# Kernel optimization log

Measured on AMD Instinct MI355X. Metric: run time of the kernel, lower is better.

The kernel has to match this reference:

```python
import jax, jax.numpy as jnp
import numpy as np

EMBED_DIM = 768
NUM_HEADS = 12
D_K = EMBED_DIM // NUM_HEADS


def setup_inputs() -> dict:
    key = jax.random.key(0)
    ks = jax.random.split(key, 9)
    b, s, d = 4, 2048, EMBED_DIM
    scale = 1.0 / np.sqrt(d)
    x = jax.random.normal(ks[0], (b, s, d), dtype=jnp.float32)
    return {
        "x": x,
        "w_q": jax.random.normal(ks[1], (d, d), dtype=jnp.float32) * scale,
        "b_q": jnp.zeros((d,), dtype=jnp.float32),
        "w_k": jax.random.normal(ks[2], (d, d), dtype=jnp.float32) * scale,
        "b_k": jnp.zeros((d,), dtype=jnp.float32),
        "w_v": jax.random.normal(ks[3], (d, d), dtype=jnp.float32) * scale,
        "b_v": jnp.zeros((d,), dtype=jnp.float32),
        "w_o": jax.random.normal(ks[4], (d, d), dtype=jnp.float32) * scale,
        "b_o": jnp.zeros((d,), dtype=jnp.float32),
    }


def reference(x, w_q, b_q, w_k, b_k, w_v, b_v, w_o, b_o):
    b, s, d = x.shape
    h, dk = NUM_HEADS, D_K
    # projections (torch Linear: x @ W^T + b)
    q = (x @ w_q.T + b_q).reshape(b, s, h, dk).transpose(0, 2, 1, 3)
    k = (x @ w_k.T + b_k).reshape(b, s, h, dk).transpose(0, 2, 1, 3)
    v = (x @ w_v.T + b_v).reshape(b, s, h, dk).transpose(0, 2, 1, 3)
    # causal attention: full [b,h,s,s] scores as in the original
    scores = jnp.einsum("bhqd,bhkd->bhqk", q, k) / jnp.sqrt(jnp.float32(dk))
    causal = jnp.tril(jnp.ones((s, s), dtype=bool))
    scores = jnp.where(causal[None, None], scores, -jnp.inf)
    attn = jax.nn.softmax(scores, axis=-1)
    out = jnp.einsum("bhqk,bhkd->bhqd", attn, v)
    out = out.transpose(0, 2, 1, 3).reshape(b, s, h * dk)
    return out @ w_o.T + b_o
```

## Files before the change

kernel.cpp:

```cpp
#include <hip/hip_runtime.h>
#include <hip/hip_bf16.h>
#include <stdint.h>

typedef short bf16x8 __attribute__((ext_vector_type(8)));
typedef float f32x4 __attribute__((ext_vector_type(4)));
typedef unsigned short u16;


__device__ __forceinline__ u16 f2bf_bits(float f) {
    __hip_bfloat16 h = __float2bfloat16(f);
    return __builtin_bit_cast(u16, h);
}

__device__ __forceinline__ uint32_t pack2bf(float a, float b) {
    uint32_t ua = __builtin_bit_cast(uint32_t, a) + 0x8000u;
    uint32_t ub = __builtin_bit_cast(uint32_t, b) + 0x8000u;
    return __builtin_amdgcn_perm(ub, ua, 0x07060302u);
}

__device__ __forceinline__ void gld_lds16(const void* g, void* l) {
    __builtin_amdgcn_global_load_lds(
        (const __attribute__((address_space(1))) void*)g,
        (__attribute__((address_space(3))) void*)l, 16, 0, 0);
}

#define CEXP 0.18033688011112042f


__global__ __launch_bounds__(256) void cast_all_kernel(
    const float* __restrict__ x, const float* __restrict__ w0,
    const float* __restrict__ w1, const float* __restrict__ w2,
    const float* __restrict__ w3, u16* __restrict__ xb,
    u16* __restrict__ o0, u16* __restrict__ o1,
    u16* __restrict__ o2, u16* __restrict__ o3,
    const float* __restrict__ bq, const float* __restrict__ bk,
    const float* __restrict__ bv, float* __restrict__ biasf) {
    int gid = blockIdx.x * 256 + threadIdx.x;
    const float* s;
    u16* d;
    int off;
    if (gid < 1572864) {
        s = x; d = xb; off = gid;
    } else {
        int g2 = gid - 1572864;
        int which = g2 / 147456;
        off = g2 - which * 147456;
        s = which == 0 ? w0 : which == 1 ? w1 : which == 2 ? w2 : w3;
        d = which == 0 ? o0 : which == 1 ? o1 : which == 2 ? o2 : o3;
    }
    float4 v = ((const float4*)s)[off];
    ushort4 u;
    u.x = f2bf_bits(v.x); u.y = f2bf_bits(v.y);
    u.z = f2bf_bits(v.z); u.w = f2bf_bits(v.w);
    ((ushort4*)d)[off] = u;
    if (gid < 2304) {
        float bb = gid < 768 ? bq[gid] : gid < 1536 ? bk[gid - 768] : bv[gid - 1536];
        biasf[gid] = bb;
    }
}


template <int RT, int MODE>
__global__ __launch_bounds__(256) void gemm_xwt(
    const u16* __restrict__ X, const u16* __restrict__ W,
    const float* __restrict__ bias, float* __restrict__ Cf,
    u16* __restrict__ Cb, u16* __restrict__ Vt, int K, int NC) {
    constexpr int JR = RT / 32;
    __shared__ u16 lsX[RT * 64];
    __shared__ u16 lsW[128 * 64];
    const int tid = threadIdx.x;
    const int w = tid >> 6, lane = tid & 63;
    const int quad = lane >> 4, l15 = lane & 15;
    const int m0 = blockIdx.y * RT, n0 = blockIdx.x * 128;
    const int wr = (w >> 1) * (RT / 2), wc = (w & 1) * 64;
    const int rr = lane >> 3, c8 = lane & 7;

    f32x4 acc[JR][4];
    for (int j = 0; j < JR; ++j)
        for (int i = 0; i < 4; ++i) acc[j][i] = (f32x4){0.f, 0.f, 0.f, 0.f};

    const int KT = K / 64;
    for (int kt = 0; kt < KT; ++kt) {
        const int k0 = kt * 64;
        __syncthreads();
        for (int cb = w; cb < RT / 8; cb += 4) {
            int row = cb * 8 + rr;
            int cg = c8 ^ ((rr ^ cb) & 7);
            gld_lds16(X + (size_t)(m0 + row) * K + k0 + cg * 8, &lsX[cb * 512]);
        }
        for (int cb = w; cb < 16; cb += 4) {
            int row = cb * 8 + rr;
            int cg = c8 ^ ((rr ^ cb) & 7);
            gld_lds16(W + (size_t)(n0 + row) * K + k0 + cg * 8, &lsW[cb * 512]);
        }
        __syncthreads();

        for (int kk = 0; kk < 2; ++kk) {
            bf16x8 xf[JR], wf[4];
            for (int j = 0; j < JR; ++j) {
                int row = wr + j * 16 + l15;
                int slot = (kk * 4 + quad) ^ ((row ^ (row >> 3)) & 7);
                xf[j] = *(const bf16x8*)&lsX[row * 64 + slot * 8];
            }
            for (int i = 0; i < 4; ++i) {
                int row = wc + i * 16 + l15;
                int slot = (kk * 4 + quad) ^ ((row ^ (row >> 3)) & 7);
                wf[i] = *(const bf16x8*)&lsW[row * 64 + slot * 8];
            }
            for (int j = 0; j < JR; ++j)
                for (int i = 0; i < 4; ++i)
                    acc[j][i] = __builtin_amdgcn_mfma_f32_16x16x32_bf16(
                        wf[i], xf[j], acc[j][i], 0, 0, 0);
        }
    }

    const bool vtile = (MODE == 2) && (n0 >= 1536);
    for (int i = 0; i < 4; ++i) {
        int c0 = n0 + wc + i * 16 + quad * 4;
        float4 bv4 = *(const float4*)&bias[c0];
        for (int j = 0; j < JR; ++j) {
            int row = m0 + wr + j * 16 + l15;
            float v0 = acc[j][i][0] + bv4.x;
            float v1 = acc[j][i][1] + bv4.y;
            float v2 = acc[j][i][2] + bv4.z;
            float v3 = acc[j][i][3] + bv4.w;
            if (MODE == 1) {
                float4 o4 = {v0, v1, v2, v3};
                *(float4*)&Cf[(size_t)row * NC + c0] = o4;
            } else if (vtile) {
                int d = c0 - 1536;
                int bq_ = row >> 11;
                int s = row & 2047;
                int h = d >> 6, dd = d & 63;
                size_t base = ((size_t)(bq_ * 12 + h) * 64 + dd) * 2048 + s;
                Vt[base]          = f2bf_bits(v0);
                Vt[base + 2048]   = f2bf_bits(v1);
                Vt[base + 4096]   = f2bf_bits(v2);
                Vt[base + 6144]   = f2bf_bits(v3);
            } else {
                uint2 pk = {pack2bf(v0, v1), pack2bf(v2, v3)};
                *(uint2*)&Cb[(size_t)row * NC + c0] = pk;
            }
        }
    }
}


__global__ __launch_bounds__(256, 3) void attn_kernel(
    const u16* __restrict__ QKV, const u16* __restrict__ Vt, u16* __restrict__ O) {
    __shared__ u16 lsQ[128 * 64];
    __shared__ u16 lsK[64 * 64];
    __shared__ u16 lsV[64 * 64];
    __shared__ u16 lsP[4][32 * 72];

    int bx = blockIdx.x;
    int bh = bx % 48;
    int qtb = 15 - (bx / 48);
    int b = bh / 12, h = bh % 12;
    int tid = threadIdx.x, w = tid >> 6, lane = tid & 63;
    int quad = lane >> 4, l15 = lane & 15;
    int rr = lane >> 3, c8 = lane & 7;

    for (int cb = w; cb < 16; cb += 4) {
        int row = cb * 8 + rr;
        int cg = c8 ^ ((rr ^ cb) & 7);
        gld_lds16(QKV + (size_t)(b * 2048 + qtb * 128 + row) * 2304 + h * 64 + cg * 8,
                  &lsQ[cb * 512]);
    }
    __syncthreads();

    bf16x8 q0[2], q1[2];
    for (int g = 0; g < 2; ++g) {
        int rowq = g * 64 + w * 16 + l15;
        int swq = (rowq ^ (rowq >> 3)) & 7;
        q0[g] = *(const bf16x8*)&lsQ[rowq * 64 + ((0 + quad) ^ swq) * 8];
        q1[g] = *(const bf16x8*)&lsQ[rowq * 64 + ((4 + quad) ^ swq) * 8];
    }

    f32x4 oacc0[4], oacc1[4];
    for (int dt = 0; dt < 4; ++dt) {
        oacc0[dt] = (f32x4){0.f, 0.f, 0.f, 0.f};
        oacc1[dt] = (f32x4){0.f, 0.f, 0.f, 0.f};
    }
    float li0 = 0.f, li1 = 0.f;
    u16* Pw = lsP[w];
    const int qrel = w * 16 + l15;
    const int ktmax = 2 * qtb + 1;

    for (int kt = 0; kt <= ktmax; ++kt) {
        __syncthreads();
        for (int cb = w; cb < 8; cb += 4) {
            int row = cb * 8 + rr;
            int cg = c8 ^ ((rr ^ cb) & 7);
            gld_lds16(QKV + (size_t)(b * 2048 + kt * 64 + row) * 2304 + 768 + h * 64 + cg * 8,
                      &lsK[cb * 512]);
            gld_lds16(Vt + (size_t)(bh * 64 + row) * 2048 + kt * 64 + cg * 8,
                      &lsV[cb * 512]);
        }
        __syncthreads();

        const bool do0 = (kt <= 2 * qtb);

        f32x4 S0[4], S1[4];
        for (int ct = 0; ct < 4; ++ct) {
            int rowk = ct * 16 + l15;
            int swk = (rowk ^ (rowk >> 3)) & 7;
            bf16x8 k0 = *(const bf16x8*)&lsK[rowk * 64 + ((0 + quad) ^ swk) * 8];
            bf16x8 k1 = *(const bf16x8*)&lsK[rowk * 64 + ((4 + quad) ^ swk) * 8];
            f32x4 z = (f32x4){0.f, 0.f, 0.f, 0.f};
            S1[ct] = __builtin_amdgcn_mfma_f32_16x16x32_bf16(k0, q0[1], z, 0, 0, 0);
            S1[ct] = __builtin_amdgcn_mfma_f32_16x16x32_bf16(k1, q1[1], S1[ct], 0, 0, 0);
            if (do0) {
                S0[ct] = __builtin_amdgcn_mfma_f32_16x16x32_bf16(k0, q0[0], z, 0, 0, 0);
                S0[ct] = __builtin_amdgcn_mfma_f32_16x16x32_bf16(k1, q1[0], S0[ct], 0, 0, 0);
            }
        }

        if (kt == 2 * qtb) {
            for (int ct = 0; ct < 4; ++ct) {
                int kbase = ct * 16 + quad * 4;
                for (int r = 0; r < 4; ++r)
                    if (kbase + r > qrel) S0[ct][r] = -1e30f;
            }
        }
        if (kt == 2 * qtb + 1) {
            for (int ct = 0; ct < 4; ++ct) {
                int kbase = ct * 16 + quad * 4;
                for (int r = 0; r < 4; ++r)
                    if (kbase + r > qrel) S1[ct][r] = -1e30f;
            }
        }

        if (do0) {
            u16* Pr = &Pw[(size_t)l15 * 72];
            for (int ct = 0; ct < 4; ++ct) {
                float p0 = __builtin_amdgcn_exp2f(S0[ct][0] * CEXP);
                float p1 = __builtin_amdgcn_exp2f(S0[ct][1] * CEXP);
                float p2 = __builtin_amdgcn_exp2f(S0[ct][2] * CEXP);
                float p3 = __builtin_amdgcn_exp2f(S0[ct][3] * CEXP);
                li0 += (p0 + p1) + (p2 + p3);
                uint2 pk = {pack2bf(p0, p1), pack2bf(p2, p3)};
                *(uint2*)&Pr[ct * 16 + quad * 4] = pk;
            }
        }
        {
            u16* Pr = &Pw[(size_t)(16 + l15) * 72];
            for (int ct = 0; ct < 4; ++ct) {
                float p0 = __builtin_amdgcn_exp2f(S1[ct][0] * CEXP);
                float p1 = __builtin_amdgcn_exp2f(S1[ct][1] * CEXP);
                float p2 = __builtin_amdgcn_exp2f(S1[ct][2] * CEXP);
                float p3 = __builtin_amdgcn_exp2f(S1[ct][3] * CEXP);
                li1 += (p0 + p1) + (p2 + p3);
                uint2 pk = {pack2bf(p0, p1), pack2bf(p2, p3)};
                *(uint2*)&Pr[ct * 16 + quad * 4] = pk;
            }
        }

        for (int ks = 0; ks < 2; ++ks) {
            bf16x8 bp1 = *(const bf16x8*)&Pw[(size_t)(16 + l15) * 72 + ks * 32 + quad * 8];
            bf16x8 bp0;
            if (do0) bp0 = *(const bf16x8*)&Pw[(size_t)l15 * 72 + ks * 32 + quad * 8];
            for (int dt = 0; dt < 4; ++dt) {
                int rowv = dt * 16 + l15;
                int swv = (rowv ^ (rowv >> 3)) & 7;
                bf16x8 av = *(const bf16x8*)&lsV[rowv * 64 + ((ks * 4 + quad) ^ swv) * 8];
                oacc1[dt] = __builtin_amdgcn_mfma_f32_16x16x32_bf16(av, bp1, oacc1[dt], 0, 0, 0);
                if (do0)
                    oacc0[dt] = __builtin_amdgcn_mfma_f32_16x16x32_bf16(av, bp0, oacc0[dt], 0, 0, 0);
            }
        }
    }

    li0 += __shfl_xor(li0, 16, 64);
    li0 += __shfl_xor(li0, 32, 64);
    li1 += __shfl_xor(li1, 16, 64);
    li1 += __shfl_xor(li1, 32, 64);
    float inv0 = 1.0f / li0, inv1 = 1.0f / li1;

    for (int g = 0; g < 2; ++g) {
        float inv = g ? inv1 : inv0;
        f32x4* oa = g ? oacc1 : oacc0;
        int row = qtb * 128 + g * 64 + w * 16 + l15;
        for (int dt = 0; dt < 4; ++dt) {
            uint2 pk = {pack2bf(oa[dt][0] * inv, oa[dt][1] * inv),
                        pack2bf(oa[dt][2] * inv, oa[dt][3] * inv)};
            *(uint2*)&O[(size_t)(b * 2048 + row) * 768 + h * 64 + dt * 16 + quad * 4] = pk;
        }
    }
}


extern "C" void kernel_launch(void* const* d_in, const int* in_sizes, int n_in,
                              void* d_out, int out_size, void* d_ws, size_t ws_size,
                              hipStream_t stream) {
    const float* x  = (const float*)d_in[0];
    const float* wq = (const float*)d_in[1];
    const float* bq = (const float*)d_in[2];
    const float* wk = (const float*)d_in[3];
    const float* bk = (const float*)d_in[4];
    const float* wv = (const float*)d_in[5];
    const float* bv = (const float*)d_in[6];
    const float* wo = (const float*)d_in[7];
    const float* bo = (const float*)d_in[8];
    float* out = (float*)d_out;

    char* ws = (char*)d_ws;
    u16*   xb    = (u16*)(ws + 0);
    u16*   Wf    = (u16*)(ws + 12582912);
    u16*   wob   = (u16*)(ws + 16121856);
    float* biasf = (float*)(ws + 17301504);
    u16*   QKVb  = (u16*)(ws + 17310720);
    u16*   Vtw   = (u16*)(ws + 55059456);
    u16*   Ow    = (u16*)(ws + 67642368);

    cast_all_kernel<<<8448, 256, 0, stream>>>(x, wq, wk, wv, wo,
                                              xb, Wf, Wf + 589824, Wf + 1179648, wob,
                                              bq, bk, bv, biasf);

    gemm_xwt<128, 2><<<dim3(18, 64), 256, 0, stream>>>(xb, Wf, biasf, nullptr, QKVb,
                                                       Vtw, 768, 2304);
    attn_kernel<<<768, 256, 0, stream>>>(QKVb, Vtw, Ow);
    gemm_xwt<64, 1><<<dim3(6, 128), 256, 0, stream>>>(Ow, wob, bo, out, nullptr,
                                                      nullptr, 768, 768);
}
```

Baseline: 219.0 us.

## Shrink attention query tile to 64 rows and overlap K/V staging with compute

```diff
diff --git a/kernel.cpp b/kernel.cpp
--- a/kernel.cpp
+++ b/kernel.cpp
@@ -146,146 +146,117 @@
 }
 
 
-__global__ __launch_bounds__(256, 3) void attn_kernel(
+__global__ __launch_bounds__(256, 5) void attn_kernel(
     const u16* __restrict__ QKV, const u16* __restrict__ Vt, u16* __restrict__ O) {
-    __shared__ u16 lsQ[128 * 64];
     __shared__ u16 lsK[64 * 64];
     __shared__ u16 lsV[64 * 64];
-    __shared__ u16 lsP[4][32 * 72];
+    __shared__ u16 lsP[4][16 * 72];
 
     int bx = blockIdx.x;
     int bh = bx % 48;
-    int qtb = 15 - (bx / 48);
-    int b = bh / 12, h = bh % 12;
+    int qt = 31 - bx / 48;
+    int bb = bh / 12, h = bh % 12;
     int tid = threadIdx.x, w = tid >> 6, lane = tid & 63;
     int quad = lane >> 4, l15 = lane & 15;
     int rr = lane >> 3, c8 = lane & 7;
 
-    for (int cb = w; cb < 16; cb += 4) {
-        int row = cb * 8 + rr;
-        int cg = c8 ^ ((rr ^ cb) & 7);
-        gld_lds16(QKV + (size_t)(b * 2048 + qtb * 128 + row) * 2304 + h * 64 + cg * 8,
-                  &lsQ[cb * 512]);
-    }
+    const size_t kgbase = (size_t)(bb * 2048) * 2304 + 768 + (size_t)h * 64;
+    const size_t vgbase = (size_t)(bh * 64) * 2048;
+
+    auto stageK = [&](int kt) {
+        for (int cb = w; cb < 8; cb += 4) {
+            int row = cb * 8 + rr;
+            int cg = c8 ^ ((rr ^ cb) & 7);
+            gld_lds16(QKV + kgbase + (size_t)(kt * 64 + row) * 2304 + cg * 8,
+                      &lsK[cb * 512]);
+        }
+    };
+    auto stageV = [&](int kt) {
+        for (int cb = w; cb < 8; cb += 4) {
+            int row = cb * 8 + rr;
+            int cg = c8 ^ ((rr ^ cb) & 7);
+            gld_lds16(Vt + vgbase + (size_t)row * 2048 + kt * 64 + cg * 8,
+                      &lsV[cb * 512]);
+        }
+    };
+
+    const int qrow = qt * 64 + w * 16 + l15;
+    const u16* qp = QKV + (size_t)(bb * 2048 + qrow) * 2304 + (size_t)h * 64;
+    bf16x8 q0 = *(const bf16x8*)(qp + quad * 8);
+    bf16x8 q1 = *(const bf16x8*)(qp + 32 + quad * 8);
+
+    stageK(0);
+    stageV(0);
     __syncthreads();
 
-    bf16x8 q0[2], q1[2];
-    for (int g = 0; g < 2; ++g) {
-        int rowq = g * 64 + w * 16 + l15;
-        int swq = (rowq ^ (rowq >> 3)) & 7;
-        q0[g] = *(const bf16x8*)&lsQ[rowq * 64 + ((0 + quad) ^ swq) * 8];
-        q1[g] = *(const bf16x8*)&lsQ[rowq * 64 + ((4 + quad) ^ swq) * 8];
-    }
-
-    f32x4 oacc0[4], oacc1[4];
-    for (int dt = 0; dt < 4; ++dt) {
-        oacc0[dt] = (f32x4){0.f, 0.f, 0.f, 0.f};
-        oacc1[dt] = (f32x4){0.f, 0.f, 0.f, 0.f};
-    }
-    float li0 = 0.f, li1 = 0.f;
+    f32x4 oacc[4];
+    for (int dt = 0; dt < 4; ++dt) oacc[dt] = (f32x4){0.f, 0.f, 0.f, 0.f};
+    float li = 0.f;
     u16* Pw = lsP[w];
     const int qrel = w * 16 + l15;
-    const int ktmax = 2 * qtb + 1;
-
-    for (int kt = 0; kt <= ktmax; ++kt) {
-        __syncthreads();
-        for (int cb = w; cb < 8; cb += 4) {
-            int row = cb * 8 + rr;
-            int cg = c8 ^ ((rr ^ cb) & 7);
-            gld_lds16(QKV + (size_t)(b * 2048 + kt * 64 + row) * 2304 + 768 + h * 64 + cg * 8,
-                      &lsK[cb * 512]);
-            gld_lds16(Vt + (size_t)(bh * 64 + row) * 2048 + kt * 64 + cg * 8,
-                      &lsV[cb * 512]);
-        }
-        __syncthreads();
-
-        const bool do0 = (kt <= 2 * qtb);
-
-        f32x4 S0[4], S1[4];
+
+    for (int kt = 0; kt <= qt; ++kt) {
+        f32x4 S[4];
+        __builtin_amdgcn_s_setprio(1);
         for (int ct = 0; ct < 4; ++ct) {
             int rowk = ct * 16 + l15;
             int swk = (rowk ^ (rowk >> 3)) & 7;
             bf16x8 k0 = *(const bf16x8*)&lsK[rowk * 64 + ((0 + quad) ^ swk) * 8];
             bf16x8 k1 = *(const bf16x8*)&lsK[rowk * 64 + ((4 + quad) ^ swk) * 8];
             f32x4 z = (f32x4){0.f, 0.f, 0.f, 0.f};
-            S1[ct] = __builtin_amdgcn_mfma_f32_16x16x32_bf16(k0, q0[1], z, 0, 0, 0);
-            S1[ct] = __builtin_amdgcn_mfma_f32_16x16x32_bf16(k1, q1[1], S1[ct], 0, 0, 0);
-            if (do0) {
-                S0[ct] = __builtin_amdgcn_mfma_f32_16x16x32_bf16(k0, q0[0], z, 0, 0, 0);
-                S0[ct] = __builtin_amdgcn_mfma_f32_16x16x32_bf16(k1, q1[0], S0[ct], 0, 0, 0);
-            }
-        }
-
-        if (kt == 2 * qtb) {
+            S[ct] = __builtin_amdgcn_mfma_f32_16x16x32_bf16(k0, q0, z, 0, 0, 0);
+            S[ct] = __builtin_amdgcn_mfma_f32_16x16x32_bf16(k1, q1, S[ct], 0, 0, 0);
+        }
+        __builtin_amdgcn_s_setprio(0);
+
+        if (kt == qt) {
             for (int ct = 0; ct < 4; ++ct) {
                 int kbase = ct * 16 + quad * 4;
                 for (int r = 0; r < 4; ++r)
-                    if (kbase + r > qrel) S0[ct][r] = -1e30f;
-            }
-        }
-        if (kt == 2 * qtb + 1) {
-            for (int ct = 0; ct < 4; ++ct) {
-                int kbase = ct * 16 + quad * 4;
-                for (int r = 0; r < 4; ++r)
-                    if (kbase + r > qrel) S1[ct][r] = -1e30f;
-            }
-        }
-
-        if (do0) {
+                    if (kbase + r > qrel) S[ct][r] = -1e30f;
+            }
+        }
+
+        {
             u16* Pr = &Pw[(size_t)l15 * 72];
             for (int ct = 0; ct < 4; ++ct) {
-                float p0 = __builtin_amdgcn_exp2f(S0[ct][0] * CEXP);
-                float p1 = __builtin_amdgcn_exp2f(S0[ct][1] * CEXP);
-                float p2 = __builtin_amdgcn_exp2f(S0[ct][2] * CEXP);
-                float p3 = __builtin_amdgcn_exp2f(S0[ct][3] * CEXP);
-                li0 += (p0 + p1) + (p2 + p3);
+                float p0 = __builtin_amdgcn_exp2f(S[ct][0] * CEXP);
+                float p1 = __builtin_amdgcn_exp2f(S[ct][1] * CEXP);
+                float p2 = __builtin_amdgcn_exp2f(S[ct][2] * CEXP);
+                float p3 = __builtin_amdgcn_exp2f(S[ct][3] * CEXP);
+                li += (p0 + p1) + (p2 + p3);
                 uint2 pk = {pack2bf(p0, p1), pack2bf(p2, p3)};
                 *(uint2*)&Pr[ct * 16 + quad * 4] = pk;
             }
         }
-        {
-            u16* Pr = &Pw[(size_t)(16 + l15) * 72];
-            for (int ct = 0; ct < 4; ++ct) {
-                float p0 = __builtin_amdgcn_exp2f(S1[ct][0] * CEXP);
-                float p1 = __builtin_amdgcn_exp2f(S1[ct][1] * CEXP);
-                float p2 = __builtin_amdgcn_exp2f(S1[ct][2] * CEXP);
-                float p3 = __builtin_amdgcn_exp2f(S1[ct][3] * CEXP);
-                li1 += (p0 + p1) + (p2 + p3);
-                uint2 pk = {pack2bf(p0, p1), pack2bf(p2, p3)};
-                *(uint2*)&Pr[ct * 16 + quad * 4] = pk;
-            }
-        }
-
+
+        __syncthreads();
+        if (kt < qt) stageK(kt + 1);
+
+        __builtin_amdgcn_s_setprio(1);
         for (int ks = 0; ks < 2; ++ks) {
-            bf16x8 bp1 = *(const bf16x8*)&Pw[(size_t)(16 + l15) * 72 + ks * 32 + quad * 8];
-            bf16x8 bp0;
-            if (do0) bp0 = *(const bf16x8*)&Pw[(size_t)l15 * 72 + ks * 32 + quad * 8];
+            bf16x8 bp = *(const bf16x8*)&Pw[(size_t)l15 * 72 + ks * 32 + quad * 8];
             for (int dt = 0; dt < 4; ++dt) {
                 int rowv = dt * 16 + l15;
                 int swv = (rowv ^ (rowv >> 3)) & 7;
                 bf16x8 av = *(const bf16x8*)&lsV[rowv * 64 + ((ks * 4 + quad) ^ swv) * 8];
-                oacc1[dt] = __builtin_amdgcn_mfma_f32_16x16x32_bf16(av, bp1, oacc1[dt], 0, 0, 0);
-                if (do0)
-                    oacc0[dt] = __builtin_amdgcn_mfma_f32_16x16x32_bf16(av, bp0, oacc0[dt], 0, 0, 0);
-            }
-        }
-    }
-
-    li0 += __shfl_xor(li0, 16, 64);
-    li0 += __shfl_xor(li0, 32, 64);
-    li1 += __shfl_xor(li1, 16, 64);
-    li1 += __shfl_xor(li1, 32, 64);
-    float inv0 = 1.0f / li0, inv1 = 1.0f / li1;
-
-    for (int g = 0; g < 2; ++g) {
-        float inv = g ? inv1 : inv0;
-        f32x4* oa = g ? oacc1 : oacc0;
-        int row = qtb * 128 + g * 64 + w * 16 + l15;
-        for (int dt = 0; dt < 4; ++dt) {
-            uint2 pk = {pack2bf(oa[dt][0] * inv, oa[dt][1] * inv),
-                        pack2bf(oa[dt][2] * inv, oa[dt][3] * inv)};
-            *(uint2*)&O[(size_t)(b * 2048 + row) * 768 + h * 64 + dt * 16 + quad * 4] = pk;
-        }
+                oacc[dt] = __builtin_amdgcn_mfma_f32_16x16x32_bf16(av, bp, oacc[dt], 0, 0, 0);
+            }
+        }
+        __builtin_amdgcn_s_setprio(0);
+
+        __syncthreads();
+        if (kt < qt) stageV(kt + 1);
+    }
+
+    li += __shfl_xor(li, 16, 64);
+    li += __shfl_xor(li, 32, 64);
+    float inv = 1.0f / li;
+
+    for (int dt = 0; dt < 4; ++dt) {
+        uint2 pk = {pack2bf(oacc[dt][0] * inv, oacc[dt][1] * inv),
+                    pack2bf(oacc[dt][2] * inv, oacc[dt][3] * inv)};
+        *(uint2*)&O[(size_t)(bb * 2048 + qrow) * 768 + h * 64 + dt * 16 + quad * 4] = pk;
     }
 }
 
@@ -319,7 +290,7 @@
 
     gemm_xwt<128, 2><<<dim3(18, 64), 256, 0, stream>>>(xb, Wf, biasf, nullptr, QKVb,
                                                        Vtw, 768, 2304);
-    attn_kernel<<<768, 256, 0, stream>>>(QKVb, Vtw, Ow);
+    attn_kernel<<<1536, 256, 0, stream>>>(QKVb, Vtw, Ow);
     gemm_xwt<64, 1><<<dim3(6, 128), 256, 0, stream>>>(Ow, wob, bo, out, nullptr,
                                                       nullptr, 768, 768);
 }
```

Result: faster. 211.5 us (-3.4%).
